# Kernel tuning notes

Measured on AMD Instinct MI355X. Metric: run time of the kernel, lower is better.

The kernel has to match this reference:

```python
import jax, jax.numpy as jnp
import numpy as np

SEQ, D_IN, D_OUT = 8192, 768, 128


def setup_inputs() -> dict:
    key = jax.random.key(0)
    k1, k2, k3, k4 = jax.random.split(key, 4)
    x = jax.random.normal(k1, (SEQ, D_IN), dtype=jnp.float32)
    # torch nn.Linear weights are stored as [d_out, d_in]
    scale = 1.0 / np.sqrt(D_IN)
    w_query = jax.random.normal(k2, (D_OUT, D_IN), dtype=jnp.float32) * scale
    w_key = jax.random.normal(k3, (D_OUT, D_IN), dtype=jnp.float32) * scale
    w_value = jax.random.normal(k4, (D_OUT, D_IN), dtype=jnp.float32) * scale
    return {"x": x, "w_query": w_query, "w_key": w_key, "w_value": w_value}


def reference(x, w_query, w_key, w_value):
    # Linear with bias=False: y = x @ W.T   (W is [d_out, d_in])
    q = x @ w_query.T                      # [N, d_out]
    k = x @ w_key.T                        # [N, d_out]
    v = x @ w_value.T                      # [N, d_out]
    inv_sqrt_d = 1.0 / jnp.sqrt(jnp.float32(k.shape[-1]))
    scores = (q @ k.T) * inv_sqrt_d        # [N, N] -- fully materialized, as in source
    weights = jax.nn.softmax(scores, axis=-1)
    return weights @ v                     # [N, d_out]
```

## Files before the change

### kernel.cpp

```cpp
#include <hip/hip_runtime.h>
#include <stdint.h>

#define SEQ 8192
#define DIN 768
#define DOUT 128

typedef __attribute__((ext_vector_type(8))) short short8;
typedef __attribute__((ext_vector_type(8))) unsigned short ushort8v;
typedef __attribute__((ext_vector_type(4))) float f32x4;

#define CEXPF (1.4426950408889634f * 0.08838834764831845f)

#if __has_builtin(__builtin_amdgcn_exp2f)
#define EXP2(x) __builtin_amdgcn_exp2f(x)
#else
#define EXP2(x) __builtin_exp2f(x)
#endif

__device__ __forceinline__ unsigned short f2bf(float f) {
  return (unsigned short)((__float_as_uint(f) + 0x8000u) >> 16);
}

__device__ __forceinline__ void gload_lds16(const void* g, void* l) {
  __builtin_amdgcn_global_load_lds(
      (const __attribute__((address_space(1))) void*)g,
      (__attribute__((address_space(3))) void*)l, 16, 0, 0);
}

#define XELEMS (SEQ * DIN)
#define WELEMS (DOUT * DIN)
__global__ void conv_kernel(const float* __restrict__ x,
                            const float* __restrict__ wq,
                            const float* __restrict__ wk,
                            const float* __restrict__ wv,
                            unsigned short* __restrict__ xb,
                            unsigned short* __restrict__ Wb) {
  int idx4 = (blockIdx.x * 256 + threadIdx.x) * 4;
  const float* src;
  unsigned short* dst;
  float sc = 1.0f;
  if (idx4 < XELEMS) {
    src = x + idx4;
    dst = xb + idx4;
  } else {
    int wi = idx4 - XELEMS;
    int z  = wi / WELEMS;
    int rem = wi - z * WELEMS;
    src = ((z == 0) ? wq : (z == 1) ? wk : wv) + rem;
    dst = Wb + wi;
    if (z == 0) sc = CEXPF;
  }
  float4 v = *(const float4*)src;
  ushort4 o;
  o.x = f2bf(v.x * sc); o.y = f2bf(v.y * sc);
  o.z = f2bf(v.z * sc); o.w = f2bf(v.w * sc);
  *(ushort4*)dst = o;
}

__launch_bounds__(256, 2)
__global__ void qkv_kernel(const unsigned short* __restrict__ xb,
                           const unsigned short* __restrict__ Wb,
                           unsigned short* __restrict__ Qb,
                           unsigned short* __restrict__ Kb,
                           unsigned short* __restrict__ Vtb) {
  __shared__ unsigned char lds_u[35072];
  unsigned char* xs = lds_u;
  unsigned char* ws = lds_u + 16384;

  const int t    = threadIdx.x;
  const int w    = t >> 6;
  const int lane = t & 63;
  const int g    = lane >> 4;
  const int r    = lane & 15;
  const int z    = blockIdx.y;
  const int m0   = blockIdx.x * 128;
  const unsigned short* Wz = Wb + (size_t)z * WELEMS;

  f32x4 acc[2][8];
#pragma unroll
  for (int i = 0; i < 2; i++)
#pragma unroll
    for (int j = 0; j < 8; j++) acc[i][j] = 0.f;

#pragma unroll 1
  for (int kb = 0; kb < DIN; kb += 64) {
#pragma unroll
    for (int c = 0; c < 4; c++) {
      int ci = (w * 4 + c) * 64 + lane;
      int row = ci >> 3, ch = ci & 7;
      int sch = ch ^ (row & 7);
      gload_lds16(xb + (size_t)(m0 + row) * DIN + kb + sch * 8,
                  xs + ((w * 4 + c) << 10) + (lane << 4));
      gload_lds16(Wz + (size_t)row * DIN + kb + sch * 8,
                  ws + ((w * 4 + c) << 10) + (lane << 4));
    }
    __syncthreads();

    short8 af[2][2], bf[2];
#pragma unroll
    for (int mt = 0; mt < 2; mt++)
#pragma unroll
      for (int kc = 0; kc < 2; kc++) {
        int row = w * 32 + mt * 16 + r;
        af[mt][kc] = *(const short8*)(ws + row * 128 + (((kc * 4 + g) ^ (r & 7)) << 4));
      }
#pragma unroll
    for (int nt = 0; nt < 8; nt++) {
      int row = nt * 16 + r;
#pragma unroll
      for (int kc = 0; kc < 2; kc++)
        bf[kc] = *(const short8*)(xs + row * 128 + (((kc * 4 + g) ^ (r & 7)) << 4));
#pragma unroll
      for (int mt = 0; mt < 2; mt++) {
        acc[mt][nt] = __builtin_amdgcn_mfma_f32_16x16x32_bf16(af[mt][0], bf[0], acc[mt][nt], 0, 0, 0);
        acc[mt][nt] = __builtin_amdgcn_mfma_f32_16x16x32_bf16(af[mt][1], bf[1], acc[mt][nt], 0, 0, 0);
      }
    }
    __syncthreads();
  }

  if (z < 2) {
    unsigned short* out = (z == 0) ? Qb : Kb;
#pragma unroll
    for (int mt = 0; mt < 2; mt++)
#pragma unroll
      for (int nt = 0; nt < 8; nt++) {
        ushort4 o;
        o.x = f2bf(acc[mt][nt][0]); o.y = f2bf(acc[mt][nt][1]);
        o.z = f2bf(acc[mt][nt][2]); o.w = f2bf(acc[mt][nt][3]);
        *(ushort4*)(out + (size_t)(m0 + nt * 16 + r) * DOUT + w * 32 + mt * 16 + g * 4) = o;
      }
  } else {
    unsigned short* ct = (unsigned short*)lds_u;
#pragma unroll
    for (int mt = 0; mt < 2; mt++)
#pragma unroll
      for (int nt = 0; nt < 8; nt++) {
        ushort4 o;
        o.x = f2bf(acc[mt][nt][0]); o.y = f2bf(acc[mt][nt][1]);
        o.z = f2bf(acc[mt][nt][2]); o.w = f2bf(acc[mt][nt][3]);
        *(ushort4*)&ct[(nt * 16 + r) * 136 + w * 32 + mt * 16 + g * 4] = o;
      }
    __syncthreads();
    int col  = t >> 1;
    int half = (t & 1) * 64;
#pragma unroll
    for (int h = 0; h < 8; h++) {
      ushort8v a;
#pragma unroll
      for (int i = 0; i < 8; i++) a[i] = ct[(half + h * 8 + i) * 136 + col];
      *(ushort8v*)(Vtb + (size_t)col * SEQ + m0 + half + h * 8) = a;
    }
  }
}

__launch_bounds__(256, 2)
__global__ void attn_kernel(const unsigned short* __restrict__ Qb,
                            const unsigned short* __restrict__ Kb,
                            const unsigned short* __restrict__ Vtb,
                            float* __restrict__ Opart,
                            float* __restrict__ lpart) {
  __shared__ unsigned char lds[51200];
  unsigned char* Kl = lds;
  unsigned char* Vl = lds + 16384;

  const int t    = threadIdx.x;
  const int wave = t >> 6;
  const int lane = t & 63;
  const int g    = lane >> 4;
  const int r    = lane & 15;
  unsigned short* Pl = (unsigned short*)(lds + 32768 + wave * 4608);

  const int qb = blockIdx.x;
  const int sp = blockIdx.y;
  const int q0 = qb * 128 + wave * 32;

  short8 qf[2][4];
#pragma unroll
  for (int nt = 0; nt < 2; nt++)
#pragma unroll
    for (int kc = 0; kc < 4; kc++)
      qf[nt][kc] = *(const short8*)(Qb + (size_t)(q0 + nt * 16 + r) * DOUT + kc * 32 + g * 8);

  short8 onesf;
#pragma unroll
  for (int j = 0; j < 8; j++) onesf[j] = (r == 0) ? (short)0x3F80 : (short)0;

  f32x4 oacc[2][8];
  f32x4 lacc[2];
#pragma unroll
  for (int st = 0; st < 2; st++) {
    lacc[st] = 0.f;
#pragma unroll
    for (int n = 0; n < 8; n++) oacc[st][n] = 0.f;
  }

#pragma unroll 1
  for (int it = 0; it < 16; it++) {
    const int kv0 = sp * 1024 + it * 64;
#pragma unroll
    for (int c = 0; c < 4; c++) {
      int idx = (wave * 4 + c) * 64 + lane;
      int krow = idx >> 4, kch = idx & 15;
      gload_lds16(Kb + ((size_t)(kv0 + krow) << 7) + ((kch ^ (krow & 15)) << 3),
                  Kl + ((wave * 4 + c) << 10) + (lane << 4));
      int d = idx >> 3, c2 = idx & 7;
      gload_lds16(Vtb + (size_t)d * SEQ + kv0 + ((c2 ^ (d & 7)) << 3),
                  Vl + ((wave * 4 + c) << 10) + (lane << 4));
    }
    __syncthreads();

    f32x4 sf[4][2];
#pragma unroll
    for (int mt = 0; mt < 4; mt++)
#pragma unroll
      for (int nt = 0; nt < 2; nt++) sf[mt][nt] = 0.f;
#pragma unroll
    for (int mt = 0; mt < 4; mt++) {
      int row = mt * 16 + r;
#pragma unroll
      for (int kc = 0; kc < 4; kc++) {
        short8 kf = *(const short8*)(Kl + row * 256 + (((kc * 4 + g) ^ (row & 15)) << 4));
        sf[mt][0] = __builtin_amdgcn_mfma_f32_16x16x32_bf16(kf, qf[0][kc], sf[mt][0], 0, 0, 0);
        sf[mt][1] = __builtin_amdgcn_mfma_f32_16x16x32_bf16(kf, qf[1][kc], sf[mt][1], 0, 0, 0);
      }
    }

#pragma unroll
    for (int mt = 0; mt < 4; mt++)
#pragma unroll
      for (int nt = 0; nt < 2; nt++) {
        ushort4 p;
        p.x = f2bf(EXP2(sf[mt][nt][0]));
        p.y = f2bf(EXP2(sf[mt][nt][1]));
        p.z = f2bf(EXP2(sf[mt][nt][2]));
        p.w = f2bf(EXP2(sf[mt][nt][3]));
        *(ushort4*)(Pl + (nt * 16 + r) * 72 + mt * 16 + g * 4) = p;
      }
    short8 pf[2][2];
#pragma unroll
    for (int st = 0; st < 2; st++)
#pragma unroll
      for (int c2 = 0; c2 < 2; c2++)
        pf[st][c2] = *(const short8*)(Pl + (st * 16 + r) * 72 + c2 * 32 + g * 8);

#pragma unroll
    for (int nt = 0; nt < 8; nt++) {
      int d = nt * 16 + r;
#pragma unroll
      for (int c2 = 0; c2 < 2; c2++) {
        short8 vf = *(const short8*)(Vl + d * 128 + (((c2 * 4 + g) ^ (d & 7)) << 4));
        oacc[0][nt] = __builtin_amdgcn_mfma_f32_16x16x32_bf16(pf[0][c2], vf, oacc[0][nt], 0, 0, 0);
        oacc[1][nt] = __builtin_amdgcn_mfma_f32_16x16x32_bf16(pf[1][c2], vf, oacc[1][nt], 0, 0, 0);
      }
    }
#pragma unroll
    for (int st = 0; st < 2; st++) {
      lacc[st] = __builtin_amdgcn_mfma_f32_16x16x32_bf16(pf[st][0], onesf, lacc[st], 0, 0, 0);
      lacc[st] = __builtin_amdgcn_mfma_f32_16x16x32_bf16(pf[st][1], onesf, lacc[st], 0, 0, 0);
    }
    __syncthreads();
  }

  const size_t pbase = (size_t)sp * SEQ;
#pragma unroll
  for (int st = 0; st < 2; st++)
#pragma unroll
    for (int rr = 0; rr < 4; rr++) {
      int qrow = q0 + st * 16 + g * 4 + rr;
#pragma unroll
      for (int nt = 0; nt < 8; nt++)
        Opart[(pbase + qrow) * DOUT + nt * 16 + r] = oacc[st][nt][rr];
      if (r == 0) lpart[pbase + qrow] = lacc[st][rr];
    }
}

__global__ void combine_kernel(const float* __restrict__ Opart,
                               const float* __restrict__ lpart,
                               float* __restrict__ out) {
  int idx = blockIdx.x * 256 + threadIdx.x;
  int s   = idx >> 5;
  int d4  = (idx & 31) * 4;
  float L = 0.f;
  f32x4 acc = 0.f;
#pragma unroll
  for (int p = 0; p < 8; p++) {
    L += lpart[p * SEQ + s];
    acc += *(const f32x4*)(Opart + ((size_t)p * SEQ + s) * DOUT + d4);
  }
  f32x4 res = acc * (1.0f / L);
  *(f32x4*)(out + (size_t)s * DOUT + d4) = res;
}

extern "C" void kernel_launch(void* const* d_in, const int* in_sizes, int n_in,
                              void* d_out, int out_size, void* d_ws, size_t ws_size,
                              hipStream_t stream) {
  const float* x  = (const float*)d_in[0];
  const float* wq = (const float*)d_in[1];
  const float* wk = (const float*)d_in[2];
  const float* wv = (const float*)d_in[3];
  float* out = (float*)d_out;

  unsigned short* Qb  = (unsigned short*)d_ws;
  unsigned short* Kb  = Qb + (size_t)SEQ * DOUT;
  unsigned short* Vtb = Kb + (size_t)SEQ * DOUT;
  float* Opart = (float*)(Vtb + (size_t)SEQ * DOUT);
  float* lpart = Opart + (size_t)8 * SEQ * DOUT;
  unsigned short* xb = (unsigned short*)Opart;
  unsigned short* Wb = xb + (size_t)XELEMS;
  if (ws_size < (size_t)(6291456 + 33554432 + 262144)) return;

  conv_kernel<<<dim3(6432), 256, 0, stream>>>(x, wq, wk, wv, xb, Wb);
  qkv_kernel<<<dim3(64, 3), 256, 0, stream>>>(xb, Wb, Qb, Kb, Vtb);
  attn_kernel<<<dim3(64, 8), 256, 0, stream>>>(Qb, Kb, Vtb, Opart, lpart);
  combine_kernel<<<dim3(1024), 256, 0, stream>>>(Opart, lpart, out);
}
```

Measured before the change: 136.9 us.

## Fuse fp32-to-bf16 conversion into QKV GEMM and widen attention per-wave query tile

Removes the separate conversion kernel by loading fp32 x and weights directly in the QKV projection, scaling and converting to bf16 in registers before writing swizzled LDS tiles. The attention kernel now uses 2 waves of 64 query rows each instead of 4 waves of 32, reusing each K and V LDS fragment across more MFMAs and using a swizzled P staging buffer. This saves a launch and a full round trip of the bf16 copy, at the cost of synchronous loads in the GEMM and much lower wave occupancy and higher register use in attention.

```diff
diff --git a/kernel.cpp b/kernel.cpp
--- a/kernel.cpp
+++ b/kernel.cpp
@@ -27,43 +27,15 @@
       (__attribute__((address_space(3))) void*)l, 16, 0, 0);
 }
 
-#define XELEMS (SEQ * DIN)
-#define WELEMS (DOUT * DIN)
-__global__ void conv_kernel(const float* __restrict__ x,
-                            const float* __restrict__ wq,
-                            const float* __restrict__ wk,
-                            const float* __restrict__ wv,
-                            unsigned short* __restrict__ xb,
-                            unsigned short* __restrict__ Wb) {
-  int idx4 = (blockIdx.x * 256 + threadIdx.x) * 4;
-  const float* src;
-  unsigned short* dst;
-  float sc = 1.0f;
-  if (idx4 < XELEMS) {
-    src = x + idx4;
-    dst = xb + idx4;
-  } else {
-    int wi = idx4 - XELEMS;
-    int z  = wi / WELEMS;
-    int rem = wi - z * WELEMS;
-    src = ((z == 0) ? wq : (z == 1) ? wk : wv) + rem;
-    dst = Wb + wi;
-    if (z == 0) sc = CEXPF;
-  }
-  float4 v = *(const float4*)src;
-  ushort4 o;
-  o.x = f2bf(v.x * sc); o.y = f2bf(v.y * sc);
-  o.z = f2bf(v.z * sc); o.w = f2bf(v.w * sc);
-  *(ushort4*)dst = o;
-}
-
 __launch_bounds__(256, 2)
-__global__ void qkv_kernel(const unsigned short* __restrict__ xb,
-                           const unsigned short* __restrict__ Wb,
+__global__ void qkv_kernel(const float* __restrict__ x,
+                           const float* __restrict__ wq,
+                           const float* __restrict__ wk,
+                           const float* __restrict__ wvp,
                            unsigned short* __restrict__ Qb,
                            unsigned short* __restrict__ Kb,
                            unsigned short* __restrict__ Vtb) {
-  __shared__ unsigned char lds_u[35072];
+  __shared__ unsigned char lds_u[34816];
   unsigned char* xs = lds_u;
   unsigned char* ws = lds_u + 16384;
 
@@ -74,25 +46,46 @@
   const int r    = lane & 15;
   const int z    = blockIdx.y;
   const int m0   = blockIdx.x * 128;
-  const unsigned short* Wz = Wb + (size_t)z * WELEMS;
+  const float* W = (z == 0) ? wq : (z == 1) ? wk : wvp;
+  const float xsc = (z == 0) ? CEXPF : 1.0f;
 
   f32x4 acc[2][8];
 #pragma unroll
   for (int i = 0; i < 2; i++)
 #pragma unroll
     for (int j = 0; j < 8; j++) acc[i][j] = 0.f;
+
+  const int trow = t >> 1;
+  const int cb   = (t & 1) * 4;
 
 #pragma unroll 1
   for (int kb = 0; kb < DIN; kb += 64) {
+    const float* xsrc = x + (size_t)(m0 + trow) * DIN + kb + cb * 8;
+    const float* wsrc = W + (size_t)trow * DIN + kb + cb * 8;
+    float4 xv[8], wv[8];
+#pragma unroll
+    for (int i = 0; i < 8; i++) {
+      xv[i] = *(const float4*)(xsrc + i * 4);
+      wv[i] = *(const float4*)(wsrc + i * 4);
+    }
+    __syncthreads();
 #pragma unroll
     for (int c = 0; c < 4; c++) {
-      int ci = (w * 4 + c) * 64 + lane;
-      int row = ci >> 3, ch = ci & 7;
-      int sch = ch ^ (row & 7);
-      gload_lds16(xb + (size_t)(m0 + row) * DIN + kb + sch * 8,
-                  xs + ((w * 4 + c) << 10) + (lane << 4));
-      gload_lds16(Wz + (size_t)row * DIN + kb + sch * 8,
-                  ws + ((w * 4 + c) << 10) + (lane << 4));
+      ushort8v xo, wo;
+#pragma unroll
+      for (int h = 0; h < 2; h++) {
+        xo[h * 4 + 0] = f2bf(xv[c * 2 + h].x * xsc);
+        xo[h * 4 + 1] = f2bf(xv[c * 2 + h].y * xsc);
+        xo[h * 4 + 2] = f2bf(xv[c * 2 + h].z * xsc);
+        xo[h * 4 + 3] = f2bf(xv[c * 2 + h].w * xsc);
+        wo[h * 4 + 0] = f2bf(wv[c * 2 + h].x);
+        wo[h * 4 + 1] = f2bf(wv[c * 2 + h].y);
+        wo[h * 4 + 2] = f2bf(wv[c * 2 + h].z);
+        wo[h * 4 + 3] = f2bf(wv[c * 2 + h].w);
+      }
+      int ch = (cb + c) ^ (trow & 7);
+      *(ushort8v*)(xs + trow * 128 + ch * 16) = xo;
+      *(ushort8v*)(ws + trow * 128 + ch * 16) = wo;
     }
     __syncthreads();
 
@@ -116,8 +109,8 @@
         acc[mt][nt] = __builtin_amdgcn_mfma_f32_16x16x32_bf16(af[mt][1], bf[1], acc[mt][nt], 0, 0, 0);
       }
     }
-    __syncthreads();
-  }
+  }
+  __syncthreads();
 
   if (z < 2) {
     unsigned short* out = (z == 0) ? Qb : Kb;
@@ -154,13 +147,13 @@
   }
 }
 
-__launch_bounds__(256, 2)
+__launch_bounds__(128, 1)
 __global__ void attn_kernel(const unsigned short* __restrict__ Qb,
                             const unsigned short* __restrict__ Kb,
                             const unsigned short* __restrict__ Vtb,
                             float* __restrict__ Opart,
                             float* __restrict__ lpart) {
-  __shared__ unsigned char lds[51200];
+  __shared__ unsigned char lds[49152];
   unsigned char* Kl = lds;
   unsigned char* Vl = lds + 16384;
 
@@ -169,15 +162,15 @@
   const int lane = t & 63;
   const int g    = lane >> 4;
   const int r    = lane & 15;
-  unsigned short* Pl = (unsigned short*)(lds + 32768 + wave * 4608);
+  unsigned char* Pl = lds + 32768 + wave * 8192;
 
   const int qb = blockIdx.x;
   const int sp = blockIdx.y;
-  const int q0 = qb * 128 + wave * 32;
-
-  short8 qf[2][4];
-#pragma unroll
-  for (int nt = 0; nt < 2; nt++)
+  const int q0 = qb * 128 + wave * 64;
+
+  short8 qf[4][4];
+#pragma unroll
+  for (int nt = 0; nt < 4; nt++)
 #pragma unroll
     for (int kc = 0; kc < 4; kc++)
       qf[nt][kc] = *(const short8*)(Qb + (size_t)(q0 + nt * 16 + r) * DOUT + kc * 32 + g * 8);
@@ -186,92 +179,99 @@
 #pragma unroll
   for (int j = 0; j < 8; j++) onesf[j] = (r == 0) ? (short)0x3F80 : (short)0;
 
-  f32x4 oacc[2][8];
-  f32x4 lacc[2];
-#pragma unroll
-  for (int st = 0; st < 2; st++) {
-    lacc[st] = 0.f;
-#pragma unroll
-    for (int n = 0; n < 8; n++) oacc[st][n] = 0.f;
+  f32x4 oacc[4][8];
+  f32x4 lacc[4];
+#pragma unroll
+  for (int nt = 0; nt < 4; nt++) {
+    lacc[nt] = 0.f;
+#pragma unroll
+    for (int d = 0; d < 8; d++) oacc[nt][d] = 0.f;
   }
 
 #pragma unroll 1
   for (int it = 0; it < 16; it++) {
     const int kv0 = sp * 1024 + it * 64;
 #pragma unroll
-    for (int c = 0; c < 4; c++) {
-      int idx = (wave * 4 + c) * 64 + lane;
+    for (int c = 0; c < 8; c++) {
+      int idx = (wave * 8 + c) * 64 + lane;
       int krow = idx >> 4, kch = idx & 15;
       gload_lds16(Kb + ((size_t)(kv0 + krow) << 7) + ((kch ^ (krow & 15)) << 3),
-                  Kl + ((wave * 4 + c) << 10) + (lane << 4));
+                  Kl + ((wave * 8 + c) << 10) + (lane << 4));
       int d = idx >> 3, c2 = idx & 7;
       gload_lds16(Vtb + (size_t)d * SEQ + kv0 + ((c2 ^ (d & 7)) << 3),
-                  Vl + ((wave * 4 + c) << 10) + (lane << 4));
-    }
-    __syncthreads();
-
-    f32x4 sf[4][2];
+                  Vl + ((wave * 8 + c) << 10) + (lane << 4));
+    }
+    __syncthreads();
+
+    f32x4 sf[4][4];
 #pragma unroll
     for (int mt = 0; mt < 4; mt++)
 #pragma unroll
-      for (int nt = 0; nt < 2; nt++) sf[mt][nt] = 0.f;
+      for (int nt = 0; nt < 4; nt++) sf[mt][nt] = 0.f;
 #pragma unroll
     for (int mt = 0; mt < 4; mt++) {
       int row = mt * 16 + r;
 #pragma unroll
       for (int kc = 0; kc < 4; kc++) {
         short8 kf = *(const short8*)(Kl + row * 256 + (((kc * 4 + g) ^ (row & 15)) << 4));
-        sf[mt][0] = __builtin_amdgcn_mfma_f32_16x16x32_bf16(kf, qf[0][kc], sf[mt][0], 0, 0, 0);
-        sf[mt][1] = __builtin_amdgcn_mfma_f32_16x16x32_bf16(kf, qf[1][kc], sf[mt][1], 0, 0, 0);
+#pragma unroll
+        for (int nt = 0; nt < 4; nt++)
+          sf[mt][nt] = __builtin_amdgcn_mfma_f32_16x16x32_bf16(kf, qf[nt][kc], sf[mt][nt], 0, 0, 0);
       }
     }
 
 #pragma unroll
     for (int mt = 0; mt < 4; mt++)
 #pragma unroll
-      for (int nt = 0; nt < 2; nt++) {
+      for (int nt = 0; nt < 4; nt++) {
         ushort4 p;
         p.x = f2bf(EXP2(sf[mt][nt][0]));
         p.y = f2bf(EXP2(sf[mt][nt][1]));
         p.z = f2bf(EXP2(sf[mt][nt][2]));
         p.w = f2bf(EXP2(sf[mt][nt][3]));
-        *(ushort4*)(Pl + (nt * 16 + r) * 72 + mt * 16 + g * 4) = p;
-      }
-    short8 pf[2][2];
-#pragma unroll
-    for (int st = 0; st < 2; st++)
-#pragma unroll
-      for (int c2 = 0; c2 < 2; c2++)
-        pf[st][c2] = *(const short8*)(Pl + (st * 16 + r) * 72 + c2 * 32 + g * 8);
-
-#pragma unroll
-    for (int nt = 0; nt < 8; nt++) {
-      int d = nt * 16 + r;
+        int q  = nt * 16 + r;
+        int ch = (2 * mt + (g >> 1)) ^ (r & 7);
+        *(ushort4*)(Pl + q * 128 + ch * 16 + (g & 1) * 8) = p;
+      }
+    short8 pf[4][2];
+#pragma unroll
+    for (int nt = 0; nt < 4; nt++)
+#pragma unroll
+      for (int c2 = 0; c2 < 2; c2++) {
+        int q = nt * 16 + r;
+        pf[nt][c2] = *(const short8*)(Pl + q * 128 + (((c2 * 4 + g) ^ (r & 7)) << 4));
+      }
+
+#pragma unroll
+    for (int dg = 0; dg < 8; dg++) {
+      int d = dg * 16 + r;
 #pragma unroll
       for (int c2 = 0; c2 < 2; c2++) {
         short8 vf = *(const short8*)(Vl + d * 128 + (((c2 * 4 + g) ^ (d & 7)) << 4));
-        oacc[0][nt] = __builtin_amdgcn_mfma_f32_16x16x32_bf16(pf[0][c2], vf, oacc[0][nt], 0, 0, 0);
-        oacc[1][nt] = __builtin_amdgcn_mfma_f32_16x16x32_bf16(pf[1][c2], vf, oacc[1][nt], 0, 0, 0);
-      }
-    }
-#pragma unroll
-    for (int st = 0; st < 2; st++) {
-      lacc[st] = __builtin_amdgcn_mfma_f32_16x16x32_bf16(pf[st][0], onesf, lacc[st], 0, 0, 0);
-      lacc[st] = __builtin_amdgcn_mfma_f32_16x16x32_bf16(pf[st][1], onesf, lacc[st], 0, 0, 0);
+#pragma unroll
+        for (int nt = 0; nt < 4; nt++)
+          oacc[nt][dg] = __builtin_amdgcn_mfma_f32_16x16x32_bf16(pf[nt][c2], vf, oacc[nt][dg], 0, 0, 0);
+      }
+    }
+#pragma unroll
+    for (int nt = 0; nt < 4; nt++) {
+      lacc[nt] = __builtin_amdgcn_mfma_f32_16x16x32_bf16(pf[nt][0], onesf, lacc[nt], 0, 0, 0);
+      lacc[nt] = __builtin_amdgcn_mfma_f32_16x16x32_bf16(pf[nt][1], onesf, lacc[nt], 0, 0, 0);
     }
     __syncthreads();
   }
 
   const size_t pbase = (size_t)sp * SEQ;
 #pragma unroll
-  for (int st = 0; st < 2; st++)
+  for (int nt = 0; nt < 4; nt++)
 #pragma unroll
     for (int rr = 0; rr < 4; rr++) {
-      int qrow = q0 + st * 16 + g * 4 + rr;
-#pragma unroll
-      for (int nt = 0; nt < 8; nt++)
-        Opart[(pbase + qrow) * DOUT + nt * 16 + r] = oacc[st][nt][rr];
-      if (r == 0) lpart[pbase + qrow] = lacc[st][rr];
+      int q = q0 + nt * 16 + g * 4 + rr;
+      float* orow = Opart + (pbase + q) * DOUT;
+#pragma unroll
+      for (int dg = 0; dg < 8; dg++)
+        orow[dg * 16 + r] = oacc[nt][dg][rr];
+      if (r == 0) lpart[pbase + q] = lacc[nt][rr];
     }
 }
 
@@ -306,12 +306,9 @@
   unsigned short* Vtb = Kb + (size_t)SEQ * DOUT;
   float* Opart = (float*)(Vtb + (size_t)SEQ * DOUT);
   float* lpart = Opart + (size_t)8 * SEQ * DOUT;
-  unsigned short* xb = (unsigned short*)Opart;
-  unsigned short* Wb = xb + (size_t)XELEMS;
   if (ws_size < (size_t)(6291456 + 33554432 + 262144)) return;
 
-  conv_kernel<<<dim3(6432), 256, 0, stream>>>(x, wq, wk, wv, xb, Wb);
-  qkv_kernel<<<dim3(64, 3), 256, 0, stream>>>(xb, Wb, Qb, Kb, Vtb);
-  attn_kernel<<<dim3(64, 8), 256, 0, stream>>>(Qb, Kb, Vtb, Opart, lpart);
+  qkv_kernel<<<dim3(64, 3), 256, 0, stream>>>(x, wq, wk, wv, Qb, Kb, Vtb);
+  attn_kernel<<<dim3(64, 8), 128, 0, stream>>>(Qb, Kb, Vtb, Opart, lpart);
   combine_kernel<<<dim3(1024), 256, 0, stream>>>(Opart, lpart, out);
 }
```

Result: slower. 165.3 us (+20.7%).

## Keep K and P in registers, double-buffer V in LDS, transpose PV MFMA

Applied to the files above, without the earlier changes.

The attention kernel now loads K fragments straight from global memory into registers rather than staging them through LDS. It also keeps the exponentiated scores in registers as MFMA operands by swapping operand order, which removes the per-wave P round-trip through LDS. V tiles are double-buffered in LDS with a new swizzle, so one barrier per iteration is enough, and the output is written with vector stores. The grid is reordered so the split index varies fastest, which may help L2 reuse of Q. The risks are higher register pressure from holding all K fragments and uncoalesced direct global K reads.

```diff
diff --git a/kernel.cpp b/kernel.cpp
--- a/kernel.cpp
+++ b/kernel.cpp
@@ -160,19 +160,16 @@
                             const unsigned short* __restrict__ Vtb,
                             float* __restrict__ Opart,
                             float* __restrict__ lpart) {
-  __shared__ unsigned char lds[51200];
-  unsigned char* Kl = lds;
-  unsigned char* Vl = lds + 16384;
+  __shared__ unsigned char Vl[2][16384];
 
   const int t    = threadIdx.x;
   const int wave = t >> 6;
   const int lane = t & 63;
   const int g    = lane >> 4;
   const int r    = lane & 15;
-  unsigned short* Pl = (unsigned short*)(lds + 32768 + wave * 4608);
-
-  const int qb = blockIdx.x;
-  const int sp = blockIdx.y;
+
+  const int sp = blockIdx.x;
+  const int qb = blockIdx.y;
   const int q0 = qb * 128 + wave * 32;
 
   short8 qf[2][4];
@@ -184,95 +181,102 @@
 
   short8 onesf;
 #pragma unroll
-  for (int j = 0; j < 8; j++) onesf[j] = (r == 0) ? (short)0x3F80 : (short)0;
+  for (int j = 0; j < 8; j++) onesf[j] = (short)0x3F80;
 
   f32x4 oacc[2][8];
   f32x4 lacc[2];
 #pragma unroll
-  for (int st = 0; st < 2; st++) {
-    lacc[st] = 0.f;
-#pragma unroll
-    for (int n = 0; n < 8; n++) oacc[st][n] = 0.f;
+  for (int nt = 0; nt < 2; nt++) {
+    lacc[nt] = 0.f;
+#pragma unroll
+    for (int dg = 0; dg < 8; dg++) oacc[nt][dg] = 0.f;
   }
 
 #pragma unroll 1
   for (int it = 0; it < 16; it++) {
     const int kv0 = sp * 1024 + it * 64;
+    unsigned char* Vb = Vl[it & 1];
+
+    short8 kf[4][4];
+#pragma unroll
+    for (int mt = 0; mt < 4; mt++)
+#pragma unroll
+      for (int kc = 0; kc < 4; kc++)
+        kf[mt][kc] = *(const short8*)(Kb + (size_t)(kv0 + mt * 16 + r) * DOUT + kc * 32 + g * 8);
+
 #pragma unroll
     for (int c = 0; c < 4; c++) {
       int idx = (wave * 4 + c) * 64 + lane;
-      int krow = idx >> 4, kch = idx & 15;
-      gload_lds16(Kb + ((size_t)(kv0 + krow) << 7) + ((kch ^ (krow & 15)) << 3),
-                  Kl + ((wave * 4 + c) << 10) + (lane << 4));
-      int d = idx >> 3, c2 = idx & 7;
-      gload_lds16(Vtb + (size_t)d * SEQ + kv0 + ((c2 ^ (d & 7)) << 3),
-                  Vl + ((wave * 4 + c) << 10) + (lane << 4));
-    }
+      int d = idx >> 3, p16 = idx & 7;
+      int c16 = p16 ^ ((d >> 1) & 7);
+      gload_lds16(Vtb + (size_t)d * SEQ + kv0 + c16 * 8,
+                  Vb + ((wave * 4 + c) << 10) + (lane << 4));
+    }
+
+    f32x4 sf[4][2];
+#pragma unroll
+    for (int mt = 0; mt < 4; mt++)
+#pragma unroll
+      for (int nt = 0; nt < 2; nt++) sf[mt][nt] = 0.f;
+#pragma unroll
+    for (int mt = 0; mt < 4; mt++)
+#pragma unroll
+      for (int kc = 0; kc < 4; kc++) {
+        sf[mt][0] = __builtin_amdgcn_mfma_f32_16x16x32_bf16(kf[mt][kc], qf[0][kc], sf[mt][0], 0, 0, 0);
+        sf[mt][1] = __builtin_amdgcn_mfma_f32_16x16x32_bf16(kf[mt][kc], qf[1][kc], sf[mt][1], 0, 0, 0);
+      }
+
+    short8 pf[2][2];
+#pragma unroll
+    for (int h = 0; h < 2; h++)
+#pragma unroll
+      for (int nt = 0; nt < 2; nt++) {
+        ushort8v p;
+#pragma unroll
+        for (int j = 0; j < 4; j++) {
+          p[j]     = f2bf(EXP2(sf[2 * h][nt][j]));
+          p[j + 4] = f2bf(EXP2(sf[2 * h + 1][nt][j]));
+        }
+        pf[h][nt] = (short8)p;
+      }
+
     __syncthreads();
 
-    f32x4 sf[4][2];
-#pragma unroll
-    for (int mt = 0; mt < 4; mt++)
-#pragma unroll
-      for (int nt = 0; nt < 2; nt++) sf[mt][nt] = 0.f;
-#pragma unroll
-    for (int mt = 0; mt < 4; mt++) {
-      int row = mt * 16 + r;
-#pragma unroll
-      for (int kc = 0; kc < 4; kc++) {
-        short8 kf = *(const short8*)(Kl + row * 256 + (((kc * 4 + g) ^ (row & 15)) << 4));
-        sf[mt][0] = __builtin_amdgcn_mfma_f32_16x16x32_bf16(kf, qf[0][kc], sf[mt][0], 0, 0, 0);
-        sf[mt][1] = __builtin_amdgcn_mfma_f32_16x16x32_bf16(kf, qf[1][kc], sf[mt][1], 0, 0, 0);
-      }
-    }
-
-#pragma unroll
-    for (int mt = 0; mt < 4; mt++)
-#pragma unroll
-      for (int nt = 0; nt < 2; nt++) {
-        ushort4 p;
-        p.x = f2bf(EXP2(sf[mt][nt][0]));
-        p.y = f2bf(EXP2(sf[mt][nt][1]));
-        p.z = f2bf(EXP2(sf[mt][nt][2]));
-        p.w = f2bf(EXP2(sf[mt][nt][3]));
-        *(ushort4*)(Pl + (nt * 16 + r) * 72 + mt * 16 + g * 4) = p;
-      }
-    short8 pf[2][2];
-#pragma unroll
-    for (int st = 0; st < 2; st++)
-#pragma unroll
-      for (int c2 = 0; c2 < 2; c2++)
-        pf[st][c2] = *(const short8*)(Pl + (st * 16 + r) * 72 + c2 * 32 + g * 8);
-
-#pragma unroll
-    for (int nt = 0; nt < 8; nt++) {
-      int d = nt * 16 + r;
-#pragma unroll
-      for (int c2 = 0; c2 < 2; c2++) {
-        short8 vf = *(const short8*)(Vl + d * 128 + (((c2 * 4 + g) ^ (d & 7)) << 4));
-        oacc[0][nt] = __builtin_amdgcn_mfma_f32_16x16x32_bf16(pf[0][c2], vf, oacc[0][nt], 0, 0, 0);
-        oacc[1][nt] = __builtin_amdgcn_mfma_f32_16x16x32_bf16(pf[1][c2], vf, oacc[1][nt], 0, 0, 0);
-      }
-    }
-#pragma unroll
-    for (int st = 0; st < 2; st++) {
-      lacc[st] = __builtin_amdgcn_mfma_f32_16x16x32_bf16(pf[st][0], onesf, lacc[st], 0, 0, 0);
-      lacc[st] = __builtin_amdgcn_mfma_f32_16x16x32_bf16(pf[st][1], onesf, lacc[st], 0, 0, 0);
-    }
-    __syncthreads();
+#pragma unroll
+    for (int dg = 0; dg < 8; dg++) {
+      int d = dg * 16 + r;
+      const unsigned char* vrow = Vb + d * 128;
+      int sw = (r >> 1) & 7;
+      int hb = (g & 1) * 8;
+#pragma unroll
+      for (int h = 0; h < 2; h++) {
+        int p16a = (4 * h + (g >> 1)) ^ sw;
+        union { uint2 u2[2]; short8 s8; } vv;
+        vv.u2[0] = *(const uint2*)(vrow + p16a * 16 + hb);
+        vv.u2[1] = *(const uint2*)(vrow + (p16a ^ 2) * 16 + hb);
+        short8 vf = vv.s8;
+#pragma unroll
+        for (int nt = 0; nt < 2; nt++)
+          oacc[nt][dg] = __builtin_amdgcn_mfma_f32_16x16x32_bf16(vf, pf[h][nt], oacc[nt][dg], 0, 0, 0);
+      }
+    }
+#pragma unroll
+    for (int nt = 0; nt < 2; nt++) {
+      lacc[nt] = __builtin_amdgcn_mfma_f32_16x16x32_bf16(onesf, pf[0][nt], lacc[nt], 0, 0, 0);
+      lacc[nt] = __builtin_amdgcn_mfma_f32_16x16x32_bf16(onesf, pf[1][nt], lacc[nt], 0, 0, 0);
+    }
   }
 
   const size_t pbase = (size_t)sp * SEQ;
 #pragma unroll
-  for (int st = 0; st < 2; st++)
-#pragma unroll
-    for (int rr = 0; rr < 4; rr++) {
-      int qrow = q0 + st * 16 + g * 4 + rr;
-#pragma unroll
-      for (int nt = 0; nt < 8; nt++)
-        Opart[(pbase + qrow) * DOUT + nt * 16 + r] = oacc[st][nt][rr];
-      if (r == 0) lpart[pbase + qrow] = lacc[st][rr];
-    }
+  for (int nt = 0; nt < 2; nt++) {
+    int q = q0 + nt * 16 + r;
+    float* orow = Opart + (pbase + q) * DOUT;
+#pragma unroll
+    for (int dg = 0; dg < 8; dg++)
+      *(f32x4*)(orow + dg * 16 + g * 4) = oacc[nt][dg];
+    if (g == 0) lpart[pbase + q] = lacc[nt][0];
+  }
 }
 
 __global__ void combine_kernel(const float* __restrict__ Opart,
@@ -312,6 +316,6 @@
 
   conv_kernel<<<dim3(6432), 256, 0, stream>>>(x, wq, wk, wv, xb, Wb);
   qkv_kernel<<<dim3(64, 3), 256, 0, stream>>>(xb, Wb, Qb, Kb, Vtb);
-  attn_kernel<<<dim3(64, 8), 256, 0, stream>>>(Qb, Kb, Vtb, Opart, lpart);
+  attn_kernel<<<dim3(8, 64), 256, 0, stream>>>(Qb, Kb, Vtb, Opart, lpart);
   combine_kernel<<<dim3(1024), 256, 0, stream>>>(Opart, lpart, out);
 }
```

Measured after the change: 168.8 us. +23.3%, slower.
